# Performance work log

Measured on AMD Instinct MI355X. Metric: run time of the kernel, lower is better.

The kernel has to match this reference:

```python
import jax, jax.numpy as jnp
import numpy as np

D = 2048      # hidden_size
H = 1408      # moe_intermediate_size
E = 8         # n_routed_experts
B, S = 2, 2048


def setup_inputs() -> dict:
    key = jax.random.key(0)
    ks = jax.random.split(key, 5)
    scale = 1.0 / np.sqrt(D)
    return {
        "hidden_states": jax.random.normal(ks[0], (B, S, D), dtype=jnp.float32),
        "Wg": jax.random.normal(ks[1], (E, D), dtype=jnp.float32) * scale,   # gate proj
        "W1": jax.random.normal(ks[2], (E, H, D), dtype=jnp.float32) * scale,  # expert gate_proj
        "W3": jax.random.normal(ks[3], (E, H, D), dtype=jnp.float32) * scale,  # expert up_proj
        "W2": jax.random.normal(ks[4], (E, D, H), dtype=jnp.float32) * (1.0 / np.sqrt(H)),  # expert down_proj
        "top_k": 2,
    }


def reference(hidden_states, Wg, W1, W3, W2, top_k):
    b, s, d = hidden_states.shape
    x = hidden_states.reshape(-1, d)                      # [T, D]
    # --- gate: softmax over expert logits, top-k selection ---
    scores = jax.nn.softmax(x @ Wg.T, axis=-1)            # [T, E]
    topk_w, topk_idx = jax.lax.top_k(scores, top_k)       # [T, K]
    # per-token combine weights over experts; zero for unselected experts
    combine = jnp.sum(jax.nn.one_hot(topk_idx, E, dtype=x.dtype) * topk_w[..., None], axis=1)  # [T, E]
    # --- experts: SwiGLU MLP, masked/weighted combine ---
    y = jnp.zeros_like(x)
    for i in range(E):
        h = jax.nn.silu(x @ W1[i].T) * (x @ W3[i].T)      # [T, H]
        y = y + combine[:, i:i + 1] * (h @ W2[i].T)       # [T, D]
    return y.reshape(b, s, d) + hidden_states
```

## Files before the change

### kernel.cpp

```cpp
#include <hip/hip_runtime.h>
#include <stdint.h>

#define DD 2048
#define HH 1408
#define EE 8
#define TT 4096

#define BM 128
#define BK 64
#define MAXBLK 72
#define NB1 22
#define NB2 16
#define NW8 2883584

using floatx4 = __attribute__((ext_vector_type(4))) float;
using bf16x8  = __attribute__((ext_vector_type(8))) __bf16;

__device__ __forceinline__ unsigned int pack_bf16(float a, float b) {
    unsigned int ua = __float_as_uint(a) + 0x8000u;
    unsigned int ub = __float_as_uint(b) + 0x8000u;
    return __builtin_amdgcn_perm(ub, ua, 0x07060302u);
}
__device__ __forceinline__ unsigned short f2bf(float a) {
    return (unsigned short)((__float_as_uint(a) + 0x8000u) >> 16);
}

__device__ __forceinline__ void gld16(const unsigned short* g, unsigned short* l) {
    __builtin_amdgcn_global_load_lds(
        (__attribute__((address_space(1))) void*)g,
        (__attribute__((address_space(3))) void*)l, 16, 0, 0);
}

__device__ __forceinline__ int xcd_swz(int bid, int live) {
    int xcd = bid & 7, pos = bid >> 3;
    int q = live >> 3, r = live & 7;
    return (xcd < r ? xcd * (q + 1) : r * (q + 1) + (xcd - r) * q) + pos;
}

__global__ __launch_bounds__(256) void k_prep(const float* __restrict__ W1,
                                              const float* __restrict__ W3,
                                              const float* __restrict__ W2,
                                              unsigned short* __restrict__ W1b,
                                              unsigned short* __restrict__ W3b,
                                              unsigned short* __restrict__ W2b,
                                              int* __restrict__ counts,
                                              int* __restrict__ cursor) {
    if (blockIdx.x == 0 && threadIdx.x < 16) {
        if (threadIdx.x < 8) counts[threadIdx.x] = 0;
        else                 cursor[threadIdx.x - 8] = 0;
    }
    int i = blockIdx.x * 256 + threadIdx.x;
    if (i >= 3 * NW8) return;
    const float* s; unsigned short* d; int off;
    if (i < NW8)          { s = W1; d = W1b; off = i; }
    else if (i < 2 * NW8) { s = W3; d = W3b; off = i - NW8; }
    else                  { s = W2; d = W2b; off = i - 2 * NW8; }
    const float4* s4 = (const float4*)s + (size_t)off * 2;
    float4 a = s4[0], b = s4[1];
    uint4 o;
    o.x = pack_bf16(a.x, a.y); o.y = pack_bf16(a.z, a.w);
    o.z = pack_bf16(b.x, b.y); o.w = pack_bf16(b.z, b.w);
    *(uint4*)(d + (size_t)off * 8) = o;
}

__global__ __launch_bounds__(256) void k_gate(const float* __restrict__ x,
                                              const float* __restrict__ Wg,
                                              unsigned short* __restrict__ Xb,
                                              float* __restrict__ out,
                                              int* __restrict__ topk_i,
                                              float* __restrict__ topk_w,
                                              int* __restrict__ counts) {
    const int t = blockIdx.x;
    const int tid = threadIdx.x;
    const float4* xr = (const float4*)(x + (size_t)t * DD);
    float4* orow = (float4*)(out + (size_t)t * DD);
    uint2* xbrow = (uint2*)(Xb + (size_t)t * DD);
    const float4* wg4 = (const float4*)Wg;
    float p[EE];
#pragma unroll
    for (int e = 0; e < EE; ++e) p[e] = 0.f;
#pragma unroll
    for (int it = 0; it < (DD / 4) / 256; ++it) {
        int d4 = it * 256 + tid;
        float4 xv = xr[d4];
        orow[d4] = xv;
        uint2 pk;
        pk.x = pack_bf16(xv.x, xv.y);
        pk.y = pack_bf16(xv.z, xv.w);
        xbrow[d4] = pk;
#pragma unroll
        for (int e = 0; e < EE; ++e) {
            float4 wv = wg4[e * (DD / 4) + d4];
            p[e] += xv.x * wv.x + xv.y * wv.y + xv.z * wv.z + xv.w * wv.w;
        }
    }
#pragma unroll
    for (int e = 0; e < EE; ++e) {
#pragma unroll
        for (int off = 32; off; off >>= 1) p[e] += __shfl_xor(p[e], off);
    }
    __shared__ float red[4][EE];
    const int wave = tid >> 6, lane = tid & 63;
    if (lane == 0) {
#pragma unroll
        for (int e = 0; e < EE; ++e) red[wave][e] = p[e];
    }
    __syncthreads();
    if (tid == 0) {
        float lg[EE];
#pragma unroll
        for (int e = 0; e < EE; ++e) lg[e] = red[0][e] + red[1][e] + red[2][e] + red[3][e];
        float mx = lg[0];
#pragma unroll
        for (int e = 1; e < EE; ++e) mx = fmaxf(mx, lg[e]);
        float den = 0.f, pr[EE];
#pragma unroll
        for (int e = 0; e < EE; ++e) { pr[e] = __expf(lg[e] - mx); den += pr[e]; }
        float inv = 1.f / den;
#pragma unroll
        for (int e = 0; e < EE; ++e) pr[e] *= inv;
        int i0 = 0; float v0 = pr[0];
#pragma unroll
        for (int e = 1; e < EE; ++e) if (pr[e] > v0) { v0 = pr[e]; i0 = e; }
        int i1 = -1; float v1 = -1.f;
#pragma unroll
        for (int e = 0; e < EE; ++e) if (e != i0 && pr[e] > v1) { v1 = pr[e]; i1 = e; }
        topk_i[t * 2 + 0] = i0; topk_i[t * 2 + 1] = i1;
        topk_w[t * 2 + 0] = v0; topk_w[t * 2 + 1] = v1;
        atomicAdd(&counts[i0], 1);
        atomicAdd(&counts[i1], 1);
    }
}

__global__ void k_scan(const int* __restrict__ counts, int* __restrict__ offs,
                       int* __restrict__ blk_e, int* __restrict__ blk_m,
                       int* __restrict__ nblk) {
    if (threadIdx.x == 0) {
        int s = 0, nb = 0;
        for (int e = 0; e < EE; ++e) {
            offs[e] = s;
            int c = counts[e];
            for (int m = 0; m < c; m += BM) { blk_e[nb] = e; blk_m[nb] = m; ++nb; }
            s += c;
        }
        *nblk = nb;
        for (int i = nb; i < MAXBLK; ++i) { blk_e[i] = 0; blk_m[i] = 0; }
    }
}

__global__ __launch_bounds__(256) void k_compact(const int* __restrict__ topk_i,
                                                 const float* __restrict__ topk_w,
                                                 const int* __restrict__ offs,
                                                 int* __restrict__ cursor,
                                                 int* __restrict__ tok_id,
                                                 float* __restrict__ tok_w) {
    const int t = blockIdx.x * 256 + threadIdx.x;
    if (t >= TT) return;
#pragma unroll
    for (int k = 0; k < 2; ++k) {
        int e = topk_i[t * 2 + k];
        int slot = atomicAdd(&cursor[e], 1);
        int p = offs[e] + slot;
        tok_id[p] = t;
        tok_w[p] = topk_w[t * 2 + k];
    }
}

__global__ __launch_bounds__(256, 3) void k_gemm1(const unsigned short* __restrict__ Xb,
                                                  const unsigned short* __restrict__ W1b,
                                                  const unsigned short* __restrict__ W3b,
                                                  const int* __restrict__ counts,
                                                  const int* __restrict__ offs,
                                                  const int* __restrict__ blk_e,
                                                  const int* __restrict__ blk_m,
                                                  const int* __restrict__ nblk,
                                                  const int* __restrict__ tok_id,
                                                  unsigned short* __restrict__ hbuf) {
    const int live = *nblk * NB1;
    int bid = blockIdx.x;
    if (bid >= live) return;
    bid = xcd_swz(bid, live);
    const int b   = bid / NB1;
    const int e   = blk_e[b];
    const int m0  = blk_m[b];
    const int cnt = counts[e];
    const int n0  = (bid % NB1) * 64;
    const int seg = offs[e];
    const int tid = threadIdx.x;

    __shared__ __align__(16) unsigned short Xs[BM * 64];
    __shared__ __align__(16) unsigned short Bs[BM * 64];
    __shared__ int ids[BM];

    if (tid < BM) ids[tid] = tok_id[seg + min(m0 + tid, cnt - 1)];
    __syncthreads();

    const int lane = tid & 63, wave = tid >> 6;
    const int lr = lane >> 3, lc = lane & 7;
    const int quad = lane >> 4, l16 = lane & 15;
    const int wm = wave >> 1, wn = wave & 1;

    const unsigned short* xp[4];
#pragma unroll
    for (int j = 0; j < 4; ++j) {
        int rl = wave * 32 + j * 8 + lr;
        xp[j] = Xb + (size_t)ids[rl] * DD + (lc ^ lr) * 8;
    }
    const unsigned short* bpp[4];
#pragma unroll
    for (int j = 0; j < 4; ++j) {
        const unsigned short* base = (j < 2) ? W1b : W3b;
        int row = n0 + wave * 16 + (j & 1) * 8 + lr;
        bpp[j] = base + ((size_t)e * HH + row) * DD + (lc ^ lr) * 8;
    }

    floatx4 acc[4][4];
#pragma unroll
    for (int i = 0; i < 4; ++i)
#pragma unroll
        for (int j = 0; j < 4; ++j) acc[i][j] = (floatx4)(0.f);

    for (int k0 = 0; k0 < DD; k0 += BK) {
#pragma unroll
        for (int j = 0; j < 4; ++j)
            gld16(xp[j] + k0, &Xs[(wave * 32 + j * 8) * 64]);
#pragma unroll
        for (int j = 0; j < 4; ++j)
            gld16(bpp[j] + k0, &Bs[(wave * 32 + j * 8) * 64]);
        __syncthreads();
#pragma unroll
        for (int kk = 0; kk < 2; ++kk) {
            bf16x8 a[4], bb[4];
#pragma unroll
            for (int mf = 0; mf < 4; ++mf) {
                int r = wm * 64 + mf * 16 + l16;
                int s = (quad + kk * 4) ^ (r & 7);
                a[mf] = *(const bf16x8*)&Xs[r * 64 + s * 8];
            }
#pragma unroll
            for (int nf = 0; nf < 4; ++nf) {
                int r = wn * 64 + nf * 16 + l16;
                int s = (quad + kk * 4) ^ (r & 7);
                bb[nf] = *(const bf16x8*)&Bs[r * 64 + s * 8];
            }
#pragma unroll
            for (int mf = 0; mf < 4; ++mf)
#pragma unroll
                for (int nf = 0; nf < 4; ++nf)
                    acc[mf][nf] = __builtin_amdgcn_mfma_f32_16x16x32_bf16(a[mf], bb[nf], acc[mf][nf], 0, 0, 0);
        }
        __syncthreads();
    }
#pragma unroll
    for (int mf = 0; mf < 4; ++mf)
#pragma unroll
        for (int reg = 0; reg < 4; ++reg) {
            int m = wm * 64 + mf * 16 + quad * 4 + reg;
            if (m0 + m < cnt) {
                size_t row = (size_t)(seg + m0 + m) * HH + n0 + wn * 32;
                float c1a = acc[mf][0][reg], c3a = acc[mf][1][reg];
                float c1b = acc[mf][2][reg], c3b = acc[mf][3][reg];
                float hva = (c1a / (1.f + __expf(-c1a))) * c3a;
                float hvb = (c1b / (1.f + __expf(-c1b))) * c3b;
                hbuf[row + l16]      = f2bf(hva);
                hbuf[row + 16 + l16] = f2bf(hvb);
            }
        }
}

__global__ __launch_bounds__(256, 3) void k_gemm2(const unsigned short* __restrict__ hbuf,
                                                  const unsigned short* __restrict__ W2b,
                                                  const int* __restrict__ counts,
                                                  const int* __restrict__ offs,
                                                  const int* __restrict__ blk_e,
                                                  const int* __restrict__ blk_m,
                                                  const int* __restrict__ nblk,
                                                  const int* __restrict__ tok_id,
                                                  const float* __restrict__ tok_w,
                                                  float* __restrict__ out) {
    const int live = *nblk * NB2;
    int bid = blockIdx.x;
    if (bid >= live) return;
    bid = xcd_swz(bid, live);
    const int b   = bid / NB2;
    const int e   = blk_e[b];
    const int m0  = blk_m[b];
    const int cnt = counts[e];
    const int n0  = (bid % NB2) * 128;
    const int seg = offs[e];
    const int tid = threadIdx.x;

    __shared__ __align__(16) unsigned short As[BM * 64];
    __shared__ __align__(16) unsigned short Bs[BM * 64];
    __shared__ int ids[BM];
    __shared__ float wts[BM];

    if (tid < BM) {
        int rc = min(m0 + tid, cnt - 1);
        ids[tid] = tok_id[seg + rc];
        wts[tid] = tok_w[seg + rc];
    }
    __syncthreads();

    const int lane = tid & 63, wave = tid >> 6;
    const int lr = lane >> 3, lc = lane & 7;
    const int quad = lane >> 4, l16 = lane & 15;
    const int wm = wave >> 1, wn = wave & 1;

    const unsigned short* ap[4];
#pragma unroll
    for (int j = 0; j < 4; ++j) {
        int rl = wave * 32 + j * 8 + lr;
        ap[j] = hbuf + (size_t)(seg + min(m0 + rl, cnt - 1)) * HH + (lc ^ lr) * 8;
    }
    const unsigned short* bp[4];
#pragma unroll
    for (int j = 0; j < 4; ++j) {
        int row = n0 + wave * 32 + j * 8 + lr;
        bp[j] = W2b + ((size_t)e * DD + row) * HH + (lc ^ lr) * 8;
    }

    floatx4 acc[4][4];
#pragma unroll
    for (int i = 0; i < 4; ++i)
#pragma unroll
        for (int j = 0; j < 4; ++j) acc[i][j] = (floatx4)(0.f);

    for (int k0 = 0; k0 < HH; k0 += BK) {
#pragma unroll
        for (int j = 0; j < 4; ++j)
            gld16(ap[j] + k0, &As[(wave * 32 + j * 8) * 64]);
#pragma unroll
        for (int j = 0; j < 4; ++j)
            gld16(bp[j] + k0, &Bs[(wave * 32 + j * 8) * 64]);
        __syncthreads();
#pragma unroll
        for (int kk = 0; kk < 2; ++kk) {
            bf16x8 a[4], bb[4];
#pragma unroll
            for (int mf = 0; mf < 4; ++mf) {
                int r = wm * 64 + mf * 16 + l16;
                int s = (quad + kk * 4) ^ (r & 7);
                a[mf] = *(const bf16x8*)&As[r * 64 + s * 8];
            }
#pragma unroll
            for (int nf = 0; nf < 4; ++nf) {
                int r = wn * 64 + nf * 16 + l16;
                int s = (quad + kk * 4) ^ (r & 7);
                bb[nf] = *(const bf16x8*)&Bs[r * 64 + s * 8];
            }
#pragma unroll
            for (int mf = 0; mf < 4; ++mf)
#pragma unroll
                for (int nf = 0; nf < 4; ++nf)
                    acc[mf][nf] = __builtin_amdgcn_mfma_f32_16x16x32_bf16(a[mf], bb[nf], acc[mf][nf], 0, 0, 0);
        }
        __syncthreads();
    }
#pragma unroll
    for (int mf = 0; mf < 4; ++mf)
#pragma unroll
        for (int reg = 0; reg < 4; ++reg) {
            int m = wm * 64 + mf * 16 + quad * 4 + reg;
            if (m0 + m < cnt) {
                int token = ids[m];
                float w = wts[m];
                float* orow = out + (size_t)token * DD + n0 + wn * 64;
#pragma unroll
                for (int nf = 0; nf < 4; ++nf)
                    atomicAdd(orow + nf * 16 + l16, w * acc[mf][nf][reg]);
            }
        }
}

extern "C" void kernel_launch(void* const* d_in, const int* in_sizes, int n_in,
                              void* d_out, int out_size, void* d_ws, size_t ws_size,
                              hipStream_t stream) {
    const float* x  = (const float*)d_in[0];
    const float* Wg = (const float*)d_in[1];
    const float* W1 = (const float*)d_in[2];
    const float* W3 = (const float*)d_in[3];
    const float* W2 = (const float*)d_in[4];
    float* out = (float*)d_out;

    int*   counts = (int*)d_ws;
    int*   cursor = counts + 8;
    int*   offs   = cursor + 8;
    int*   blk_e  = offs + 8;
    int*   blk_m  = blk_e + MAXBLK;
    int*   nblk   = blk_m + MAXBLK;
    int*   topk_i = nblk + 8;
    float* topk_w = (float*)(topk_i + 2 * TT);
    int*   tok_id = (int*)(topk_w + 2 * TT);
    float* tok_w  = (float*)(tok_id + 2 * TT);
    unsigned short* hbuf = (unsigned short*)(tok_w + 2 * TT);
    unsigned short* Xb   = hbuf + (size_t)2 * TT * HH;
    unsigned short* W1b  = Xb + (size_t)TT * DD;
    unsigned short* W3b  = W1b + (size_t)EE * HH * DD;
    unsigned short* W2b  = W3b + (size_t)EE * HH * DD;

    k_prep<<<(3 * NW8) / 256, 256, 0, stream>>>(W1, W3, W2, W1b, W3b, W2b, counts, cursor);
    k_gate<<<TT, 256, 0, stream>>>(x, Wg, Xb, out, topk_i, topk_w, counts);
    k_scan<<<1, 64, 0, stream>>>(counts, offs, blk_e, blk_m, nblk);
    k_compact<<<TT / 256, 256, 0, stream>>>(topk_i, topk_w, offs, cursor, tok_id, tok_w);
    k_gemm1<<<MAXBLK * NB1, 256, 0, stream>>>(Xb, W1b, W3b, counts, offs,
                                              blk_e, blk_m, nblk, tok_id, hbuf);
    k_gemm2<<<MAXBLK * NB2, 256, 0, stream>>>(hbuf, W2b, counts, offs,
                                              blk_e, blk_m, nblk, tok_id, tok_w, out);
}
```

Before: 687.2 us.

## Double-buffer LDS tiles in both expert GEMMs to overlap loads with MFMA

Both grouped GEMM kernels now keep two LDS buffers and issue global-to-LDS loads two k-tiles ahead. Each iteration reads all fragments into registers, hits one barrier, starts the next prefetch, and then runs the MFMAs at raised wave priority. Synchronisation uses manual vmcnt/lgkmcnt waits and raw barriers instead of two __syncthreads per tile. The goal is to hide global load latency behind matrix math. In exchange LDS use doubles and launch bounds drop from 3 to 2 blocks per CU, so occupancy falls.

New measurement: 692.2 us. Within noise of the previous version (+0.7%).

```diff
diff --git a/kernel.cpp b/kernel.cpp
--- a/kernel.cpp
+++ b/kernel.cpp
@@ -166,7 +166,7 @@
     }
 }
 
-__global__ __launch_bounds__(256, 3) void k_gemm1(const unsigned short* __restrict__ Xb,
+__global__ __launch_bounds__(256, 2) void k_gemm1(const unsigned short* __restrict__ Xb,
                                                   const unsigned short* __restrict__ W1b,
                                                   const unsigned short* __restrict__ W3b,
                                                   const int* __restrict__ counts,
@@ -188,8 +188,8 @@
     const int seg = offs[e];
     const int tid = threadIdx.x;
 
-    __shared__ __align__(16) unsigned short Xs[BM * 64];
-    __shared__ __align__(16) unsigned short Bs[BM * 64];
+    __shared__ __align__(16) unsigned short Xs[2][BM * 64];
+    __shared__ __align__(16) unsigned short Bs[2][BM * 64];
     __shared__ int ids[BM];
 
     if (tid < BM) ids[tid] = tok_id[seg + min(m0 + tid, cnt - 1)];
@@ -220,36 +220,59 @@
 #pragma unroll
         for (int j = 0; j < 4; ++j) acc[i][j] = (floatx4)(0.f);
 
-    for (int k0 = 0; k0 < DD; k0 += BK) {
+    auto stage = [&](int buf, int k0) {
 #pragma unroll
         for (int j = 0; j < 4; ++j)
-            gld16(xp[j] + k0, &Xs[(wave * 32 + j * 8) * 64]);
+            gld16(xp[j] + k0, &Xs[buf][(wave * 32 + j * 8) * 64]);
 #pragma unroll
         for (int j = 0; j < 4; ++j)
-            gld16(bpp[j] + k0, &Bs[(wave * 32 + j * 8) * 64]);
-        __syncthreads();
+            gld16(bpp[j] + k0, &Bs[buf][(wave * 32 + j * 8) * 64]);
+    };
+
+    const int NT = DD / BK;
+    stage(0, 0);
+    stage(1, BK);
+    asm volatile("s_waitcnt vmcnt(8)" ::: "memory");
+    __builtin_amdgcn_s_barrier();
+    __builtin_amdgcn_sched_barrier(0);
+
+    int cur = 0;
+    for (int t = 0; t < NT; ++t) {
+        bf16x8 a[4][2], bb[4][2];
 #pragma unroll
         for (int kk = 0; kk < 2; ++kk) {
-            bf16x8 a[4], bb[4];
 #pragma unroll
             for (int mf = 0; mf < 4; ++mf) {
                 int r = wm * 64 + mf * 16 + l16;
                 int s = (quad + kk * 4) ^ (r & 7);
-                a[mf] = *(const bf16x8*)&Xs[r * 64 + s * 8];
+                a[mf][kk] = *(const bf16x8*)&Xs[cur][r * 64 + s * 8];
             }
 #pragma unroll
             for (int nf = 0; nf < 4; ++nf) {
                 int r = wn * 64 + nf * 16 + l16;
                 int s = (quad + kk * 4) ^ (r & 7);
-                bb[nf] = *(const bf16x8*)&Bs[r * 64 + s * 8];
-            }
+                bb[nf][kk] = *(const bf16x8*)&Bs[cur][r * 64 + s * 8];
+            }
+        }
+        asm volatile("s_waitcnt lgkmcnt(0)" ::: "memory");
+        __builtin_amdgcn_sched_barrier(0);
+        __builtin_amdgcn_s_barrier();
+        __builtin_amdgcn_sched_barrier(0);
+        if (t + 2 < NT) stage(cur, (t + 2) * BK);
+        __builtin_amdgcn_s_setprio(1);
+#pragma unroll
+        for (int kk = 0; kk < 2; ++kk)
 #pragma unroll
             for (int mf = 0; mf < 4; ++mf)
 #pragma unroll
                 for (int nf = 0; nf < 4; ++nf)
-                    acc[mf][nf] = __builtin_amdgcn_mfma_f32_16x16x32_bf16(a[mf], bb[nf], acc[mf][nf], 0, 0, 0);
-        }
-        __syncthreads();
+                    acc[mf][nf] = __builtin_amdgcn_mfma_f32_16x16x32_bf16(a[mf][kk], bb[nf][kk], acc[mf][nf], 0, 0, 0);
+        __builtin_amdgcn_s_setprio(0);
+        if (t + 2 < NT) asm volatile("s_waitcnt vmcnt(8)" ::: "memory");
+        else            asm volatile("s_waitcnt vmcnt(0)" ::: "memory");
+        __builtin_amdgcn_s_barrier();
+        __builtin_amdgcn_sched_barrier(0);
+        cur ^= 1;
     }
 #pragma unroll
     for (int mf = 0; mf < 4; ++mf)
@@ -268,7 +291,7 @@
         }
 }
 
-__global__ __launch_bounds__(256, 3) void k_gemm2(const unsigned short* __restrict__ hbuf,
+__global__ __launch_bounds__(256, 2) void k_gemm2(const unsigned short* __restrict__ hbuf,
                                                   const unsigned short* __restrict__ W2b,
                                                   const int* __restrict__ counts,
                                                   const int* __restrict__ offs,
@@ -290,8 +313,8 @@
     const int seg = offs[e];
     const int tid = threadIdx.x;
 
-    __shared__ __align__(16) unsigned short As[BM * 64];
-    __shared__ __align__(16) unsigned short Bs[BM * 64];
+    __shared__ __align__(16) unsigned short As[2][BM * 64];
+    __shared__ __align__(16) unsigned short Bs[2][BM * 64];
     __shared__ int ids[BM];
     __shared__ float wts[BM];
 
@@ -326,36 +349,59 @@
 #pragma unroll
         for (int j = 0; j < 4; ++j) acc[i][j] = (floatx4)(0.f);
 
-    for (int k0 = 0; k0 < HH; k0 += BK) {
+    auto stage = [&](int buf, int k0) {
 #pragma unroll
         for (int j = 0; j < 4; ++j)
-            gld16(ap[j] + k0, &As[(wave * 32 + j * 8) * 64]);
+            gld16(ap[j] + k0, &As[buf][(wave * 32 + j * 8) * 64]);
 #pragma unroll
         for (int j = 0; j < 4; ++j)
-            gld16(bp[j] + k0, &Bs[(wave * 32 + j * 8) * 64]);
-        __syncthreads();
+            gld16(bp[j] + k0, &Bs[buf][(wave * 32 + j * 8) * 64]);
+    };
+
+    const int NT = HH / BK;
+    stage(0, 0);
+    stage(1, BK);
+    asm volatile("s_waitcnt vmcnt(8)" ::: "memory");
+    __builtin_amdgcn_s_barrier();
+    __builtin_amdgcn_sched_barrier(0);
+
+    int cur = 0;
+    for (int t = 0; t < NT; ++t) {
+        bf16x8 a[4][2], bb[4][2];
 #pragma unroll
         for (int kk = 0; kk < 2; ++kk) {
-            bf16x8 a[4], bb[4];
 #pragma unroll
             for (int mf = 0; mf < 4; ++mf) {
                 int r = wm * 64 + mf * 16 + l16;
                 int s = (quad + kk * 4) ^ (r & 7);
-                a[mf] = *(const bf16x8*)&As[r * 64 + s * 8];
+                a[mf][kk] = *(const bf16x8*)&As[cur][r * 64 + s * 8];
             }
 #pragma unroll
             for (int nf = 0; nf < 4; ++nf) {
                 int r = wn * 64 + nf * 16 + l16;
                 int s = (quad + kk * 4) ^ (r & 7);
-                bb[nf] = *(const bf16x8*)&Bs[r * 64 + s * 8];
-            }
+                bb[nf][kk] = *(const bf16x8*)&Bs[cur][r * 64 + s * 8];
+            }
+        }
+        asm volatile("s_waitcnt lgkmcnt(0)" ::: "memory");
+        __builtin_amdgcn_sched_barrier(0);
+        __builtin_amdgcn_s_barrier();
+        __builtin_amdgcn_sched_barrier(0);
+        if (t + 2 < NT) stage(cur, (t + 2) * BK);
+        __builtin_amdgcn_s_setprio(1);
+#pragma unroll
+        for (int kk = 0; kk < 2; ++kk)
 #pragma unroll
             for (int mf = 0; mf < 4; ++mf)
 #pragma unroll
                 for (int nf = 0; nf < 4; ++nf)
-                    acc[mf][nf] = __builtin_amdgcn_mfma_f32_16x16x32_bf16(a[mf], bb[nf], acc[mf][nf], 0, 0, 0);
-        }
-        __syncthreads();
+                    acc[mf][nf] = __builtin_amdgcn_mfma_f32_16x16x32_bf16(a[mf][kk], bb[nf][kk], acc[mf][nf], 0, 0, 0);
+        __builtin_amdgcn_s_setprio(0);
+        if (t + 2 < NT) asm volatile("s_waitcnt vmcnt(8)" ::: "memory");
+        else            asm volatile("s_waitcnt vmcnt(0)" ::: "memory");
+        __builtin_amdgcn_s_barrier();
+        __builtin_amdgcn_sched_barrier(0);
+        cur ^= 1;
     }
 #pragma unroll
     for (int mf = 0; mf < 4; ++mf)
```

## Fuse fp32-to-bf16 weight conversion into expert GEMMs with double-buffered pipeline

Applied to the files above, without the earlier changes.

Drops the separate weight-conversion prep kernel. The expert GEMMs now read fp32 weights directly into registers, pack them to bf16 and write them to a double-buffered LDS tile, with prefetch several tiles ahead and MFMA priority hints. This removes a full pass that read all fp32 weights and wrote bf16 copies, but each GEMM block now reads fp32 weights, which is twice the bytes per tile, and every M-block converts them again. Occupancy drops from 3 to 2 blocks per CU because of the extra registers and LDS.

Result: no change. 678.3 us (-1.3%).

```diff
diff --git a/kernel.cpp b/kernel.cpp
--- a/kernel.cpp
+++ b/kernel.cpp
@@ -11,7 +11,6 @@
 #define MAXBLK 72
 #define NB1 22
 #define NB2 16
-#define NW8 2883584
 
 using floatx4 = __attribute__((ext_vector_type(4))) float;
 using bf16x8  = __attribute__((ext_vector_type(8))) __bf16;
@@ -37,31 +36,72 @@
     return (xcd < r ? xcd * (q + 1) : r * (q + 1) + (xcd - r) * q) + pos;
 }
 
-__global__ __launch_bounds__(256) void k_prep(const float* __restrict__ W1,
-                                              const float* __restrict__ W3,
-                                              const float* __restrict__ W2,
-                                              unsigned short* __restrict__ W1b,
-                                              unsigned short* __restrict__ W3b,
-                                              unsigned short* __restrict__ W2b,
-                                              int* __restrict__ counts,
-                                              int* __restrict__ cursor) {
-    if (blockIdx.x == 0 && threadIdx.x < 16) {
-        if (threadIdx.x < 8) counts[threadIdx.x] = 0;
-        else                 cursor[threadIdx.x - 8] = 0;
-    }
-    int i = blockIdx.x * 256 + threadIdx.x;
-    if (i >= 3 * NW8) return;
-    const float* s; unsigned short* d; int off;
-    if (i < NW8)          { s = W1; d = W1b; off = i; }
-    else if (i < 2 * NW8) { s = W3; d = W3b; off = i - NW8; }
-    else                  { s = W2; d = W2b; off = i - 2 * NW8; }
-    const float4* s4 = (const float4*)s + (size_t)off * 2;
-    float4 a = s4[0], b = s4[1];
-    uint4 o;
-    o.x = pack_bf16(a.x, a.y); o.y = pack_bf16(a.z, a.w);
-    o.z = pack_bf16(b.x, b.y); o.w = pack_bf16(b.z, b.w);
-    *(uint4*)(d + (size_t)off * 8) = o;
-}
+#define FRAGS(CUR)                                                                   \
+    _Pragma("unroll")                                                                \
+    for (int kk = 0; kk < 2; ++kk) {                                                 \
+        _Pragma("unroll")                                                            \
+        for (int mf = 0; mf < 4; ++mf) {                                             \
+            int r = wm * 64 + mf * 16 + l16; int s = (quad + kk * 4) ^ (r & 7);      \
+            a[mf][kk] = *(const bf16x8*)&Xs[CUR][r * 64 + s * 8]; }                  \
+        _Pragma("unroll")                                                            \
+        for (int nf = 0; nf < 4; ++nf) {                                             \
+            int r = wn * 64 + nf * 16 + l16; int s = (quad + kk * 4) ^ (r & 7);      \
+            bb[nf][kk] = *(const bf16x8*)&Bs[CUR][r * 64 + s * 8]; } }
+
+#define MFMA_CLUSTER                                                                 \
+    __builtin_amdgcn_s_setprio(1);                                                   \
+    _Pragma("unroll")                                                                \
+    for (int kk = 0; kk < 2; ++kk)                                                   \
+    { _Pragma("unroll")                                                              \
+      for (int mf = 0; mf < 4; ++mf)                                                 \
+      { _Pragma("unroll")                                                            \
+        for (int nf = 0; nf < 4; ++nf)                                               \
+            acc[mf][nf] = __builtin_amdgcn_mfma_f32_16x16x32_bf16(                   \
+                a[mf][kk], bb[nf][kk], acc[mf][nf], 0, 0, 0); } }                    \
+    __builtin_amdgcn_s_setprio(0);
+
+#define WLOAD(P, K0)                                                                 \
+    { _Pragma("unroll")                                                              \
+      for (int j = 0; j < 4; ++j) {                                                  \
+          const float* s_ = wsrc[j] + (K0);                                          \
+          wr[8 * (P) + 2 * j]     = *(const float4*)s_;                              \
+          wr[8 * (P) + 2 * j + 1] = *(const float4*)(s_ + 4); } }
+
+#define WWRITE(P, CUR)                                                               \
+    { _Pragma("unroll")                                                              \
+      for (int j = 0; j < 4; ++j) {                                                  \
+          float4 u = wr[8 * (P) + 2 * j], v = wr[8 * (P) + 2 * j + 1];               \
+          uint4 o;                                                                   \
+          o.x = pack_bf16(u.x, u.y); o.y = pack_bf16(u.z, u.w);                      \
+          o.z = pack_bf16(v.x, v.y); o.w = pack_bf16(v.z, v.w);                      \
+          int rl = wave * 32 + j * 8 + lr;                                           \
+          *(uint4*)&Bs[CUR][rl * 64 + (lc ^ lr) * 8] = o; } }
+
+#define XSTAGE(CUR, K0)                                                              \
+    { _Pragma("unroll")                                                              \
+      for (int j = 0; j < 4; ++j)                                                    \
+          gld16(xp[j] + (K0), &Xs[CUR][(wave * 32 + j * 8) * 64]); }
+
+#define BARMID                                                                       \
+    asm volatile("s_waitcnt lgkmcnt(0)" ::: "memory");                               \
+    __builtin_amdgcn_sched_barrier(0);                                               \
+    __builtin_amdgcn_s_barrier();                                                    \
+    __builtin_amdgcn_sched_barrier(0);
+
+#define BAREND(N)                                                                    \
+    asm volatile("s_waitcnt vmcnt(" #N ") lgkmcnt(0)" ::: "memory");                 \
+    __builtin_amdgcn_sched_barrier(0);                                               \
+    __builtin_amdgcn_s_barrier();                                                    \
+    __builtin_amdgcn_sched_barrier(0);
+
+#define MAIN_ITER(CUR, P, TT)                                                        \
+    FRAGS(CUR)                                                                       \
+    BARMID                                                                           \
+    WWRITE(P, CUR)                                                                   \
+    WLOAD(P, ((TT) + 4) * BK)                                                        \
+    XSTAGE(CUR, ((TT) + 2) * BK)                                                     \
+    MFMA_CLUSTER                                                                     \
+    BAREND(12)
 
 __global__ __launch_bounds__(256) void k_gate(const float* __restrict__ x,
                                               const float* __restrict__ Wg,
@@ -166,9 +206,9 @@
     }
 }
 
-__global__ __launch_bounds__(256, 3) void k_gemm1(const unsigned short* __restrict__ Xb,
-                                                  const unsigned short* __restrict__ W1b,
-                                                  const unsigned short* __restrict__ W3b,
+__global__ __launch_bounds__(256, 2) void k_gemm1(const unsigned short* __restrict__ Xb,
+                                                  const float* __restrict__ W1f,
+                                                  const float* __restrict__ W3f,
                                                   const int* __restrict__ counts,
                                                   const int* __restrict__ offs,
                                                   const int* __restrict__ blk_e,
@@ -188,8 +228,8 @@
     const int seg = offs[e];
     const int tid = threadIdx.x;
 
-    __shared__ __align__(16) unsigned short Xs[BM * 64];
-    __shared__ __align__(16) unsigned short Bs[BM * 64];
+    __shared__ __align__(16) unsigned short Xs[2][BM * 64];
+    __shared__ __align__(16) unsigned short Bs[2][BM * 64];
     __shared__ int ids[BM];
 
     if (tid < BM) ids[tid] = tok_id[seg + min(m0 + tid, cnt - 1)];
@@ -206,12 +246,12 @@
         int rl = wave * 32 + j * 8 + lr;
         xp[j] = Xb + (size_t)ids[rl] * DD + (lc ^ lr) * 8;
     }
-    const unsigned short* bpp[4];
+    const float* wsrc[4];
 #pragma unroll
     for (int j = 0; j < 4; ++j) {
-        const unsigned short* base = (j < 2) ? W1b : W3b;
+        const float* base = (j < 2) ? W1f : W3f;
         int row = n0 + wave * 16 + (j & 1) * 8 + lr;
-        bpp[j] = base + ((size_t)e * HH + row) * DD + (lc ^ lr) * 8;
+        wsrc[j] = base + ((size_t)e * HH + row) * DD + lc * 8;
     }
 
     floatx4 acc[4][4];
@@ -220,37 +260,32 @@
 #pragma unroll
         for (int j = 0; j < 4; ++j) acc[i][j] = (floatx4)(0.f);
 
-    for (int k0 = 0; k0 < DD; k0 += BK) {
-#pragma unroll
-        for (int j = 0; j < 4; ++j)
-            gld16(xp[j] + k0, &Xs[(wave * 32 + j * 8) * 64]);
-#pragma unroll
-        for (int j = 0; j < 4; ++j)
-            gld16(bpp[j] + k0, &Bs[(wave * 32 + j * 8) * 64]);
-        __syncthreads();
-#pragma unroll
-        for (int kk = 0; kk < 2; ++kk) {
-            bf16x8 a[4], bb[4];
-#pragma unroll
-            for (int mf = 0; mf < 4; ++mf) {
-                int r = wm * 64 + mf * 16 + l16;
-                int s = (quad + kk * 4) ^ (r & 7);
-                a[mf] = *(const bf16x8*)&Xs[r * 64 + s * 8];
-            }
-#pragma unroll
-            for (int nf = 0; nf < 4; ++nf) {
-                int r = wn * 64 + nf * 16 + l16;
-                int s = (quad + kk * 4) ^ (r & 7);
-                bb[nf] = *(const bf16x8*)&Bs[r * 64 + s * 8];
-            }
-#pragma unroll
-            for (int mf = 0; mf < 4; ++mf)
-#pragma unroll
-                for (int nf = 0; nf < 4; ++nf)
-                    acc[mf][nf] = __builtin_amdgcn_mfma_f32_16x16x32_bf16(a[mf], bb[nf], acc[mf][nf], 0, 0, 0);
-        }
-        __syncthreads();
-    }
+    float4 wr[16];
+    bf16x8 a[4][2], bb[4][2];
+
+    const int NT = DD / BK;
+    WLOAD(0, 0) WLOAD(1, BK)
+    asm volatile("s_waitcnt vmcnt(0)" ::: "memory");
+    __builtin_amdgcn_sched_barrier(0);
+    WWRITE(0, 0) WWRITE(1, 1)
+    WLOAD(0, 2 * BK)
+    XSTAGE(0, 0)
+    WLOAD(1, 3 * BK)
+    XSTAGE(1, BK)
+    BAREND(12)
+
+    for (int t = 0; t < NT - 4; t += 2) {
+        MAIN_ITER(0, 0, t)
+        MAIN_ITER(1, 1, t + 1)
+    }
+    FRAGS(0) BARMID WWRITE(0, 0) XSTAGE(0, (NT - 2) * BK) MFMA_CLUSTER BAREND(4)
+    FRAGS(1) BARMID WWRITE(1, 1) XSTAGE(1, (NT - 1) * BK) MFMA_CLUSTER BAREND(0)
+    FRAGS(0) BARMID MFMA_CLUSTER BAREND(0)
+    FRAGS(1)
+    asm volatile("s_waitcnt lgkmcnt(0)" ::: "memory");
+    __builtin_amdgcn_sched_barrier(0);
+    MFMA_CLUSTER
+
 #pragma unroll
     for (int mf = 0; mf < 4; ++mf)
 #pragma unroll
@@ -268,8 +303,8 @@
         }
 }
 
-__global__ __launch_bounds__(256, 3) void k_gemm2(const unsigned short* __restrict__ hbuf,
-                                                  const unsigned short* __restrict__ W2b,
+__global__ __launch_bounds__(256, 2) void k_gemm2(const unsigned short* __restrict__ hbuf,
+                                                  const float* __restrict__ W2f,
                                                   const int* __restrict__ counts,
                                                   const int* __restrict__ offs,
                                                   const int* __restrict__ blk_e,
@@ -290,8 +325,8 @@
     const int seg = offs[e];
     const int tid = threadIdx.x;
 
-    __shared__ __align__(16) unsigned short As[BM * 64];
-    __shared__ __align__(16) unsigned short Bs[BM * 64];
+    __shared__ __align__(16) unsigned short Xs[2][BM * 64];
+    __shared__ __align__(16) unsigned short Bs[2][BM * 64];
     __shared__ int ids[BM];
     __shared__ float wts[BM];
 
@@ -307,17 +342,17 @@
     const int quad = lane >> 4, l16 = lane & 15;
     const int wm = wave >> 1, wn = wave & 1;
 
-    const unsigned short* ap[4];
+    const unsigned short* xp[4];
 #pragma unroll
     for (int j = 0; j < 4; ++j) {
         int rl = wave * 32 + j * 8 + lr;
-        ap[j] = hbuf + (size_t)(seg + min(m0 + rl, cnt - 1)) * HH + (lc ^ lr) * 8;
-    }
-    const unsigned short* bp[4];
+        xp[j] = hbuf + (size_t)(seg + min(m0 + rl, cnt - 1)) * HH + (lc ^ lr) * 8;
+    }
+    const float* wsrc[4];
 #pragma unroll
     for (int j = 0; j < 4; ++j) {
         int row = n0 + wave * 32 + j * 8 + lr;
-        bp[j] = W2b + ((size_t)e * DD + row) * HH + (lc ^ lr) * 8;
+        wsrc[j] = W2f + ((size_t)e * DD + row) * HH + lc * 8;
     }
 
     floatx4 acc[4][4];
@@ -326,37 +361,32 @@
 #pragma unroll
         for (int j = 0; j < 4; ++j) acc[i][j] = (floatx4)(0.f);
 
-    for (int k0 = 0; k0 < HH; k0 += BK) {
-#pragma unroll
-        for (int j = 0; j < 4; ++j)
-            gld16(ap[j] + k0, &As[(wave * 32 + j * 8) * 64]);
-#pragma unroll
-        for (int j = 0; j < 4; ++j)
-            gld16(bp[j] + k0, &Bs[(wave * 32 + j * 8) * 64]);
-        __syncthreads();
-#pragma unroll
-        for (int kk = 0; kk < 2; ++kk) {
-            bf16x8 a[4], bb[4];
-#pragma unroll
-            for (int mf = 0; mf < 4; ++mf) {
-                int r = wm * 64 + mf * 16 + l16;
-                int s = (quad + kk * 4) ^ (r & 7);
-                a[mf] = *(const bf16x8*)&As[r * 64 + s * 8];
-            }
-#pragma unroll
-            for (int nf = 0; nf < 4; ++nf) {
-                int r = wn * 64 + nf * 16 + l16;
-                int s = (quad + kk * 4) ^ (r & 7);
-                bb[nf] = *(const bf16x8*)&Bs[r * 64 + s * 8];
-            }
-#pragma unroll
-            for (int mf = 0; mf < 4; ++mf)
-#pragma unroll
-                for (int nf = 0; nf < 4; ++nf)
-                    acc[mf][nf] = __builtin_amdgcn_mfma_f32_16x16x32_bf16(a[mf], bb[nf], acc[mf][nf], 0, 0, 0);
-        }
-        __syncthreads();
-    }
+    float4 wr[16];
+    bf16x8 a[4][2], bb[4][2];
+
+    const int NT = HH / BK;
+    WLOAD(0, 0) WLOAD(1, BK)
+    asm volatile("s_waitcnt vmcnt(0)" ::: "memory");
+    __builtin_amdgcn_sched_barrier(0);
+    WWRITE(0, 0) WWRITE(1, 1)
+    WLOAD(0, 2 * BK)
+    XSTAGE(0, 0)
+    WLOAD(1, 3 * BK)
+    XSTAGE(1, BK)
+    BAREND(12)
+
+    for (int t = 0; t < NT - 4; t += 2) {
+        MAIN_ITER(0, 0, t)
+        MAIN_ITER(1, 1, t + 1)
+    }
+    FRAGS(0) BARMID WWRITE(0, 0) XSTAGE(0, (NT - 2) * BK) MFMA_CLUSTER BAREND(4)
+    FRAGS(1) BARMID WWRITE(1, 1) XSTAGE(1, (NT - 1) * BK) MFMA_CLUSTER BAREND(0)
+    FRAGS(0) BARMID MFMA_CLUSTER BAREND(0)
+    FRAGS(1)
+    asm volatile("s_waitcnt lgkmcnt(0)" ::: "memory");
+    __builtin_amdgcn_sched_barrier(0);
+    MFMA_CLUSTER
+
 #pragma unroll
     for (int mf = 0; mf < 4; ++mf)
 #pragma unroll
@@ -395,16 +425,13 @@
     float* tok_w  = (float*)(tok_id + 2 * TT);
     unsigned short* hbuf = (unsigned short*)(tok_w + 2 * TT);
     unsigned short* Xb   = hbuf + (size_t)2 * TT * HH;
-    unsigned short* W1b  = Xb + (size_t)TT * DD;
-    unsigned short* W3b  = W1b + (size_t)EE * HH * DD;
-    unsigned short* W2b  = W3b + (size_t)EE * HH * DD;
-
-    k_prep<<<(3 * NW8) / 256, 256, 0, stream>>>(W1, W3, W2, W1b, W3b, W2b, counts, cursor);
+
+    hipMemsetAsync(counts, 0, 16 * sizeof(int), stream);
     k_gate<<<TT, 256, 0, stream>>>(x, Wg, Xb, out, topk_i, topk_w, counts);
     k_scan<<<1, 64, 0, stream>>>(counts, offs, blk_e, blk_m, nblk);
     k_compact<<<TT / 256, 256, 0, stream>>>(topk_i, topk_w, offs, cursor, tok_id, tok_w);
-    k_gemm1<<<MAXBLK * NB1, 256, 0, stream>>>(Xb, W1b, W3b, counts, offs,
+    k_gemm1<<<MAXBLK * NB1, 256, 0, stream>>>(Xb, W1, W3, counts, offs,
                                               blk_e, blk_m, nblk, tok_id, hbuf);
-    k_gemm2<<<MAXBLK * NB2, 256, 0, stream>>>(hbuf, W2b, counts, offs,
+    k_gemm2<<<MAXBLK * NB2, 256, 0, stream>>>(hbuf, W2, counts, offs,
                                               blk_e, blk_m, nblk, tok_id, tok_w, out);
 }
```
